# Performance work log

Measured on AMD Instinct MI355X. Metric: run time of the kernel, lower is better.

## Reference

```python
import jax, jax.numpy as jnp
import numpy as np

B, N, D_IN, D_OUT = 8, 256, 128, 128


def setup_inputs() -> dict:
    key = jax.random.key(0)
    k1, k2, k3, k4, k5 = jax.random.split(key, 5)
    hidden = jax.random.normal(k1, (B, N, D_IN), dtype=jnp.float32)
    adj = jax.random.uniform(k2, (B, N, N), dtype=jnp.float32)
    dep_embed = jax.random.normal(k3, (B, N, N, D_IN), dtype=jnp.float32)
    weight = jax.random.normal(k4, (D_IN, D_OUT), dtype=jnp.float32) * 0.05
    bias_weight = jax.random.normal(k5, (D_OUT,), dtype=jnp.float32) * 0.05
    return {"hidden": hidden, "adj": adj, "dep_embed": dep_embed,
            "weight": weight, "bias_weight": bias_weight}


def reference(hidden, adj, dep_embed, weight, bias_weight):
    # fusion[b,p,q,d] = (hidden[b,p] + dep_embed[b,p,q]) @ W   (broadcast instead of tile)
    fusion = jnp.einsum('bpqe,ed->bpqd', hidden[:, :, None, :] + dep_embed, weight)
    # out[b,i,d] = sum_j adj[b,i,j] * fusion[b,j,i,d]   (transpose+mask+reduce fused)
    out = jnp.einsum('bij,bjid->bid', adj, fusion)
    return out + bias_weight
```

## Files before the change

kernel.cpp:

```cpp
#include <hip/hip_runtime.h>


constexpr int Bc = 8;
constexpr int Nc = 256;
constexpr int Dc = 128;

__global__ __launch_bounds__(256, 2) void depgcn_kernel(
    const float* __restrict__ hidden,
    const float* __restrict__ adj,
    const float* __restrict__ dep,
    const float* __restrict__ W,
    const float* __restrict__ bias,
    float* __restrict__ out)
{
    const int bi = blockIdx.x;
    const int b  = bi >> 8;
    const int i  = bi & (Nc - 1);
    const int t  = threadIdx.x;
    const int g  = t >> 5;
    const int c  = t & 31;

    __shared__ float sAdj[Nc];
    __shared__ float sP[8][Dc];
    __shared__ float sT[Dc];
    __shared__ float sO[2][Dc];

    sAdj[t] = adj[((size_t)b * Nc + i) * Nc + t];
    __syncthreads();

    const float* depP = dep + (((size_t)b * Nc) * Nc + i) * Dc + (size_t)c * 4;
    const float* hidP = hidden + ((size_t)b * Nc) * Dc + (size_t)c * 4;

    float4 acc = make_float4(0.f, 0.f, 0.f, 0.f);
    #pragma unroll 4
    for (int j = g; j < Nc; j += 8) {
        const float  a  = sAdj[j];
        const float4 d4 = *(const float4*)(depP + (size_t)j * Nc * Dc);
        const float4 h4 = *(const float4*)(hidP + (size_t)j * Dc);
        acc.x = fmaf(a, d4.x + h4.x, acc.x);
        acc.y = fmaf(a, d4.y + h4.y, acc.y);
        acc.z = fmaf(a, d4.z + h4.z, acc.z);
        acc.w = fmaf(a, d4.w + h4.w, acc.w);
    }
    *(float4*)&sP[g][c * 4] = acc;
    __syncthreads();

    if (t < Dc) {
        float s = 0.f;
        #pragma unroll
        for (int gg = 0; gg < 8; ++gg) s += sP[gg][t];
        sT[t] = s;
    }
    __syncthreads();

    {
        const int d = t & (Dc - 1);
        const int h = t >> 7;
        const float* wp = W + (size_t)(h * 64) * Dc + d;
        float s = 0.f;
        #pragma unroll 8
        for (int e = 0; e < 64; ++e)
            s = fmaf(sT[h * 64 + e], wp[(size_t)e * Dc], s);
        sO[h][d] = s;
    }
    __syncthreads();

    if (t < Dc) {
        out[((size_t)b * Nc + i) * Dc + t] = sO[0][t] + sO[1][t] + bias[t];
    }
}

extern "C" void kernel_launch(void* const* d_in, const int* in_sizes, int n_in,
                              void* d_out, int out_size, void* d_ws, size_t ws_size,
                              hipStream_t stream) {
    const float* hidden = (const float*)d_in[0];
    const float* adj    = (const float*)d_in[1];
    const float* dep    = (const float*)d_in[2];
    const float* W      = (const float*)d_in[3];
    const float* bias   = (const float*)d_in[4];
    float* out          = (float*)d_out;

    depgcn_kernel<<<dim3(Bc * Nc), dim3(256), 0, stream>>>(hidden, adj, dep, W, bias, out);
}
```

Baseline: 363.0 us.

## Split into chunked partial-sum kernel with contiguous dep reads and reduce-project kernel

Splits the work into two kernels. The first tiles over blocks of 32 output rows and 16 j values, so each j step reads a 4 KB contiguous dep span instead of a 512 B strided one, and it stages hidden and adj in shared memory. Per-chunk partial sums go to a workspace buffer. The second kernel reduces the 16 partials and applies W and the bias. This trades an extra launch and about 16 MB of workspace traffic for better DRAM locality on the dominant dep stream.

```diff
diff --git a/kernel.cpp b/kernel.cpp
--- a/kernel.cpp
+++ b/kernel.cpp
@@ -1,14 +1,79 @@
 #include <hip/hip_runtime.h>
 
 
-constexpr int Bc = 8;
-constexpr int Nc = 256;
-constexpr int Dc = 128;
+constexpr int Bc  = 8;
+constexpr int Nc  = 256;
+constexpr int Dc  = 128;
+constexpr int JC  = 16;
+constexpr int NCH = Nc / JC;
+constexpr int IT  = 32;
+constexpr int NIQ = Nc / IT;
 
-__global__ __launch_bounds__(256, 2) void depgcn_kernel(
+__global__ __launch_bounds__(256) void depgcn_k1(
     const float* __restrict__ hidden,
     const float* __restrict__ adj,
     const float* __restrict__ dep,
+    float* __restrict__ P)
+{
+    const int blk = blockIdx.x;
+    const int iq  = blk & (NIQ - 1);
+    const int jc  = (blk >> 3) & (NCH - 1);
+    const int b   = blk >> 7;
+    const int t   = threadIdx.x;
+    const int g   = t >> 5;
+    const int c   = t & 31;
+
+    __shared__ float sH[JC][Dc];
+    __shared__ float sA[IT][JC];
+
+    {
+        const int row = t >> 4;
+        const int col = (t & 15) * 8;
+        const float* hp = hidden + ((size_t)b * Nc + jc * JC + row) * Dc + col;
+        *(float4*)&sH[row][col]     = *(const float4*)hp;
+        *(float4*)&sH[row][col + 4] = *(const float4*)(hp + 4);
+    }
+    {
+        const int iL = t >> 3;
+        const int jL = (t & 7) * 2;
+        const float* ap = adj + ((size_t)b * Nc + iq * IT + iL) * Nc + jc * JC + jL;
+        sA[iL][jL]     = ap[0];
+        sA[iL][jL + 1] = ap[1];
+    }
+    __syncthreads();
+
+    float4 acc[4];
+    #pragma unroll
+    for (int ii = 0; ii < 4; ++ii) acc[ii] = make_float4(0.f, 0.f, 0.f, 0.f);
+
+    const float* depB = dep +
+        ((((size_t)b * Nc + jc * JC) * Nc) + iq * IT + g * 4) * Dc + (size_t)c * 4;
+
+    #pragma unroll 2
+    for (int j = 0; j < JC; ++j) {
+        const float4 h4 = *(const float4*)&sH[j][c * 4];
+        const float* dj = depB + (size_t)j * Nc * Dc;
+        #pragma unroll
+        for (int ii = 0; ii < 4; ++ii) {
+            const float  a  = sA[g * 4 + ii][j];
+            const float4 d4 = *(const float4*)(dj + (size_t)ii * Dc);
+            acc[ii].x = fmaf(a, d4.x + h4.x, acc[ii].x);
+            acc[ii].y = fmaf(a, d4.y + h4.y, acc[ii].y);
+            acc[ii].z = fmaf(a, d4.z + h4.z, acc[ii].z);
+            acc[ii].w = fmaf(a, d4.w + h4.w, acc[ii].w);
+        }
+    }
+
+    #pragma unroll
+    for (int ii = 0; ii < 4; ++ii) {
+        const int ig = iq * IT + g * 4 + ii;
+        float* pp = P + (((size_t)b * Nc + ig) * NCH + jc) * Dc + (size_t)c * 4;
+        *(float4*)pp = acc[ii];
+    }
+}
+
+__global__ __launch_bounds__(256) void depgcn_k2(
+    const float* __restrict__ P,
     const float* __restrict__ W,
     const float* __restrict__ bias,
     float* __restrict__ out)
@@ -17,38 +82,15 @@
     const int b  = bi >> 8;
     const int i  = bi & (Nc - 1);
     const int t  = threadIdx.x;
-    const int g  = t >> 5;
-    const int c  = t & 31;
 
-    __shared__ float sAdj[Nc];
-    __shared__ float sP[8][Dc];
     __shared__ float sT[Dc];
     __shared__ float sO[2][Dc];
 
-    sAdj[t] = adj[((size_t)b * Nc + i) * Nc + t];
-    __syncthreads();
-
-    const float* depP = dep + (((size_t)b * Nc) * Nc + i) * Dc + (size_t)c * 4;
-    const float* hidP = hidden + ((size_t)b * Nc) * Dc + (size_t)c * 4;
-
-    float4 acc = make_float4(0.f, 0.f, 0.f, 0.f);
-    #pragma unroll 4
-    for (int j = g; j < Nc; j += 8) {
-        const float  a  = sAdj[j];
-        const float4 d4 = *(const float4*)(depP + (size_t)j * Nc * Dc);
-        const float4 h4 = *(const float4*)(hidP + (size_t)j * Dc);
-        acc.x = fmaf(a, d4.x + h4.x, acc.x);
-        acc.y = fmaf(a, d4.y + h4.y, acc.y);
-        acc.z = fmaf(a, d4.z + h4.z, acc.z);
-        acc.w = fmaf(a, d4.w + h4.w, acc.w);
-    }
-    *(float4*)&sP[g][c * 4] = acc;
-    __syncthreads();
-
     if (t < Dc) {
+        const float* pp = P + ((size_t)b * Nc + i) * NCH * Dc + t;
         float s = 0.f;
         #pragma unroll
-        for (int gg = 0; gg < 8; ++gg) s += sP[gg][t];
+        for (int ch = 0; ch < NCH; ++ch) s += pp[(size_t)ch * Dc];
         sT[t] = s;
     }
     __syncthreads();
@@ -79,6 +121,8 @@
     const float* W      = (const float*)d_in[3];
     const float* bias   = (const float*)d_in[4];
     float* out          = (float*)d_out;
+    float* P            = (float*)d_ws;
 
-    depgcn_kernel<<<dim3(Bc * Nc), dim3(256), 0, stream>>>(hidden, adj, dep, W, bias, out);
+    depgcn_k1<<<dim3(Bc * NCH * NIQ), dim3(256), 0, stream>>>(hidden, adj, dep, P);
+    depgcn_k2<<<dim3(Bc * Nc), dim3(256), 0, stream>>>(P, W, bias, out);
 }
```

Measured after the change: 374.2 us. 1.03x slower.

## Process eight output rows per block with batched nontemporal dep loads

Applied to the files above, without the earlier changes.

Each block now handles eight consecutive i rows (one warp per row) instead of one row, so the grid shrinks from 2048 to 256 blocks. Each warp walks all j itself, issuing eight nontemporal dep loads at once before using them, and neighbouring warps read adjacent dep rows so their accesses share contiguous memory. The cross-group reduction step and its syncs are removed, and the projection through W is done per warp with four outputs per lane. The risk is that 256 blocks may not fill the GPU well and each warp now runs a longer serial j loop.

```diff
diff --git a/kernel.cpp b/kernel.cpp
--- a/kernel.cpp
+++ b/kernel.cpp
@@ -4,8 +4,12 @@
 constexpr int Bc = 8;
 constexpr int Nc = 256;
 constexpr int Dc = 128;
+constexpr int IT = 8;
+constexpr int NIQ = Nc / IT;
 
-__global__ __launch_bounds__(256, 2) void depgcn_kernel(
+typedef float floatx4 __attribute__((ext_vector_type(4)));
+
+__global__ void depgcn_kernel(
     const float* __restrict__ hidden,
     const float* __restrict__ adj,
     const float* __restrict__ dep,
@@ -13,60 +17,66 @@
     const float* __restrict__ bias,
     float* __restrict__ out)
 {
-    const int bi = blockIdx.x;
-    const int b  = bi >> 8;
-    const int i  = bi & (Nc - 1);
-    const int t  = threadIdx.x;
-    const int g  = t >> 5;
-    const int c  = t & 31;
+    const int blk = blockIdx.x;
+    const int iq  = blk & (NIQ - 1);
+    const int b   = blk >> 5;
+    const int i0  = iq * IT;
+    const int t   = threadIdx.x;
+    const int iL  = t >> 5;
+    const int c   = t & 31;
 
-    __shared__ float sAdj[Nc];
-    __shared__ float sP[8][Dc];
-    __shared__ float sT[Dc];
-    __shared__ float sO[2][Dc];
+    __shared__ float sAdj[IT][Nc];
+    __shared__ float sT[IT][Dc];
 
-    sAdj[t] = adj[((size_t)b * Nc + i) * Nc + t];
-    __syncthreads();
-
-    const float* depP = dep + (((size_t)b * Nc) * Nc + i) * Dc + (size_t)c * 4;
-    const float* hidP = hidden + ((size_t)b * Nc) * Dc + (size_t)c * 4;
-
-    float4 acc = make_float4(0.f, 0.f, 0.f, 0.f);
-    #pragma unroll 4
-    for (int j = g; j < Nc; j += 8) {
-        const float  a  = sAdj[j];
-        const float4 d4 = *(const float4*)(depP + (size_t)j * Nc * Dc);
-        const float4 h4 = *(const float4*)(hidP + (size_t)j * Dc);
-        acc.x = fmaf(a, d4.x + h4.x, acc.x);
-        acc.y = fmaf(a, d4.y + h4.y, acc.y);
-        acc.z = fmaf(a, d4.z + h4.z, acc.z);
-        acc.w = fmaf(a, d4.w + h4.w, acc.w);
-    }
-    *(float4*)&sP[g][c * 4] = acc;
-    __syncthreads();
-
-    if (t < Dc) {
-        float s = 0.f;
-        #pragma unroll
-        for (int gg = 0; gg < 8; ++gg) s += sP[gg][t];
-        sT[t] = s;
+    {
+        const int r  = t >> 5;
+        const int cc = (t & 31) * 8;
+        const float* ap = adj + ((size_t)b * Nc + i0 + r) * Nc + cc;
+        *(floatx4*)&sAdj[r][cc]     = *(const floatx4*)ap;
+        *(floatx4*)&sAdj[r][cc + 4] = *(const floatx4*)(ap + 4);
     }
     __syncthreads();
 
-    {
-        const int d = t & (Dc - 1);
-        const int h = t >> 7;
-        const float* wp = W + (size_t)(h * 64) * Dc + d;
-        float s = 0.f;
-        #pragma unroll 8
-        for (int e = 0; e < 64; ++e)
-            s = fmaf(sT[h * 64 + e], wp[(size_t)e * Dc], s);
-        sO[h][d] = s;
+    const float* depP = dep + (((size_t)b * Nc) * Nc + i0 + iL) * Dc + (size_t)c * 4;
+    const float* hidP = hidden + ((size_t)b * Nc) * Dc + (size_t)c * 4;
+
+    floatx4 acc = {0.f, 0.f, 0.f, 0.f};
+
+    for (int j0 = 0; j0 < Nc; j0 += 8) {
+        floatx4 d[8], h[8];
+        #pragma unroll
+        for (int k = 0; k < 8; ++k)
+            d[k] = __builtin_nontemporal_load(
+                (const floatx4*)(depP + (size_t)(j0 + k) * Nc * Dc));
+        #pragma unroll
+        for (int k = 0; k < 8; ++k)
+            h[k] = *(const floatx4*)(hidP + (size_t)(j0 + k) * Dc);
+        #pragma unroll
+        for (int k = 0; k < 8; ++k) {
+            const float a = sAdj[iL][j0 + k];
+            acc += a * (d[k] + h[k]);
+        }
     }
+
+    *(floatx4*)&sT[iL][c * 4] = acc;
     __syncthreads();
 
-    if (t < Dc) {
-        out[((size_t)b * Nc + i) * Dc + t] = sO[0][t] + sO[1][t] + bias[t];
+    {
+        float s0 = bias[c], s1 = bias[c + 32], s2 = bias[c + 64], s3 = bias[c + 96];
+        #pragma unroll 8
+        for (int e = 0; e < Dc; ++e) {
+            const float te = sT[iL][e];
+            const float* wr = W + (size_t)e * Dc;
+            s0 = fmaf(te, wr[c],      s0);
+            s1 = fmaf(te, wr[c + 32], s1);
+            s2 = fmaf(te, wr[c + 64], s2);
+            s3 = fmaf(te, wr[c + 96], s3);
+        }
+        float* op = out + ((size_t)b * Nc + i0 + iL) * Dc;
+        op[c]      = s0;
+        op[c + 32] = s1;
+        op[c + 64] = s2;
+        op[c + 96] = s3;
     }
 }
 
@@ -80,5 +90,5 @@
     const float* bias   = (const float*)d_in[4];
     float* out          = (float*)d_out;
 
-    depgcn_kernel<<<dim3(Bc * Nc), dim3(256), 0, stream>>>(hidden, adj, dep, W, bias, out);
+    depgcn_kernel<<<dim3(Bc * NIQ), dim3(256), 0, stream>>>(hidden, adj, dep, W, bias, out);
 }
```

Measured after the change: 383.0 us. 5.5% more time.
